# Kernel tuning notes

Measured on AMD Instinct MI355X. Metric: run time of the kernel, lower is better.

## Reference

```python
import jax, jax.numpy as jnp
import numpy as np

H, D = 2, 128            # heads, per-head dim
F_OUT = H * D            # out_channels = 256
N_ADD = 20000
N_DEL = 20000
E = 200000
N_SEL = 4096


def setup_inputs() -> dict:
    key = jax.random.key(0)
    ks = jax.random.split(key, 24)
    p = lambda k, shp: (jax.random.normal(k, shp, dtype=jnp.float32) * 0.05)
    inp = {
        "x_add": jax.random.normal(ks[0], (N_ADD, 768), dtype=jnp.float32),
        "x_del": jax.random.normal(ks[1], (N_DEL, 768), dtype=jnp.float32),
        # per-node-type projections (torch Linear: W [out,in], b [out])
        "W_add": p(ks[2], (F_OUT, 768)), "b_add": p(ks[3], (F_OUT,)),
        "W_del": p(ks[4], (F_OUT, 768)), "b_del": p(ks[5], (F_OUT,)),
        # per-edge-type attention vectors [H, D]
        "att_ad_s": p(ks[6], (H, D)), "att_ad_d": p(ks[7], (H, D)),
        "att_da_s": p(ks[8], (H, D)), "att_da_d": p(ks[9], (H, D)),
        "att_aa_s": p(ks[10], (H, D)), "att_aa_d": p(ks[11], (H, D)),
        "att_dd_s": p(ks[12], (H, D)), "att_dd_d": p(ks[13], (H, D)),
        # semantic attention: k_lin Linear(F_OUT->F_OUT) and query q [F_OUT]
        "k_W": p(ks[14], (F_OUT, F_OUT)), "k_b": p(ks[15], (F_OUT,)),
        "q": p(ks[16], (F_OUT,)),
        # edge indices: row 0 = src node ids, row 1 = dst node ids
        "ei_ad": jax.random.randint(ks[17], (2, E), 0, N_ADD),
        "ei_da": jax.random.randint(ks[18], (2, E), 0, N_DEL),
        "ei_aa": jax.random.randint(ks[19], (2, E), 0, N_ADD),
        "ei_dd": jax.random.randint(ks[20], (2, E), 0, N_DEL),
        "del_idx": jax.random.randint(ks[21], (N_SEL,), 0, N_DEL),
    }
    return inp


def _seg_softmax(a, seg, n):
    # numerically-stable softmax over edges grouped by destination node
    m = jax.ops.segment_max(a, seg, num_segments=n)
    m = jnp.where(jnp.isfinite(m), m, 0.0)
    e = jnp.exp(a - m[seg])
    s = jax.ops.segment_sum(e, seg, num_segments=n)
    return e / (s[seg] + 1e-16)


def _edge_attn(x_src, x_dst, att_s, att_d, ei, n_dst):
    # x_*: [N, H, D]; GAT-style additive attention with leaky_relu(0.2)
    a_s = (x_src * att_s).sum(-1)                   # [Ns, H]
    a_d = (x_dst * att_d).sum(-1)                   # [Nd, H]
    alpha = jax.nn.leaky_relu(a_s[ei[0]] + a_d[ei[1]], 0.2)  # [E, H]
    alpha = _seg_softmax(alpha, ei[1], n_dst)       # [E, H]
    msg = x_src[ei[0]] * alpha[:, :, None]          # [E, H, D]
    out = jax.ops.segment_sum(msg, ei[1], num_segments=n_dst)  # [Nd, H, D]
    return jax.nn.relu(out).reshape(n_dst, F_OUT)


def _group(xs, q, k_W, k_b):
    # semantic (metapath-level) attention
    out = jnp.stack(xs)                              # [M, N, F]
    score = (q * jnp.tanh(out @ k_W.T + k_b).mean(axis=1)).sum(-1)  # [M]
    attn = jax.nn.softmax(score)
    return (attn[:, None, None] * out).sum(0)        # [N, F]


def reference(x_add, x_del, W_add, b_add, W_del, b_del,
              att_ad_s, att_ad_d, att_da_s, att_da_d,
              att_aa_s, att_aa_d, att_dd_s, att_dd_d,
              k_W, k_b, q, ei_ad, ei_da, ei_aa, ei_dd, del_idx):
    ha = (x_add @ W_add.T + b_add).reshape(N_ADD, H, D)
    hd = (x_del @ W_del.T + b_del).reshape(N_DEL, H, D)
    # messages grouped by destination node type
    out_del_ad = _edge_attn(ha, hd, att_ad_s, att_ad_d, ei_ad, N_DEL)
    out_del_dd = _edge_attn(hd, hd, att_dd_s, att_dd_d, ei_dd, N_DEL)
    out_add_da = _edge_attn(hd, ha, att_da_s, att_da_d, ei_da, N_ADD)
    out_add_aa = _edge_attn(ha, ha, att_aa_s, att_aa_d, ei_aa, N_ADD)
    out_del = _group([out_del_ad, out_del_dd], q, k_W, k_b)
    _ = _group([out_add_da, out_add_aa], q, k_W, k_b)  # computed by HANConv, unused downstream
    return out_del[del_idx]  # index_select on del_node
```

## Files before the change

kernel.cpp:

```cpp
#include <hip/hip_runtime.h>
#include <hip/hip_bf16.h>


typedef unsigned short u16;
typedef __attribute__((ext_vector_type(8))) __bf16 bf16x8;
typedef __attribute__((ext_vector_type(4))) float f32x4;
typedef const __attribute__((address_space(1))) unsigned int* gu32p;
typedef __attribute__((address_space(3))) unsigned int* su32p;

__device__ inline float bf2f(u16 u) {
    union { unsigned int i; float f; } c; c.i = ((unsigned int)u) << 16; return c.f;
}
__device__ inline u16 f2bf(float f) {
    union { float f; unsigned int i; } c; c.f = f;
    return (u16)((c.i + 0x7fffu + ((c.i >> 16) & 1u)) >> 16);
}
__device__ inline bf16x8 cvt8(f32x4 a, f32x4 b) {
    bf16x8 r;
    r[0] = (__bf16)a[0]; r[1] = (__bf16)a[1]; r[2] = (__bf16)a[2]; r[3] = (__bf16)a[3];
    r[4] = (__bf16)b[0]; r[5] = (__bf16)b[1]; r[6] = (__bf16)b[2]; r[7] = (__bf16)b[3];
    return r;
}
__device__ inline float fast_tanh(float x) {
    x = fminf(9.f, fmaxf(-9.f, x));
    float t = __expf(2.f * x);
    return (t - 1.f) / (t + 1.f);
}

__global__ __launch_bounds__(256) void prep_count(const float* __restrict__ W0, u16* __restrict__ wb0,
                                                  const float* __restrict__ W1, u16* __restrict__ wb1,
                                                  const float* __restrict__ kW, u16* __restrict__ kwb,
                                                  const int* __restrict__ eiA, int* __restrict__ cntA,
                                                  const int* __restrict__ eiB, int* __restrict__ cntB, int E) {
    int b = blockIdx.x;
    if (b < 224) {
        int idx = b * 256 + threadIdx.x;
        const float* s; u16* d; int i;
        if (idx < 24576)      { s = W0; d = wb0; i = idx; }
        else if (idx < 49152) { s = W1; d = wb1; i = idx - 24576; }
        else                  { s = kW; d = kwb; i = idx - 49152; }
        int e = i * 8;
        *(bf16x8*)(d + e) = cvt8(*(const f32x4*)(s + e), *(const f32x4*)(s + e + 4));
    } else {
        int idx = (b - 224) * 256 + threadIdx.x;
        int which = idx >= E;
        int e = idx - (which ? E : 0);
        if (e >= E) return;
        const int* ei = which ? eiB : eiA;
        int* cnt = which ? cntB : cntA;
        atomicAdd(&cnt[ei[E + e]], 1);
    }
}

__global__ __launch_bounds__(256) void gemm_h2(
    const float* __restrict__ X0, const u16* __restrict__ Wb0,
    const float* __restrict__ b0, u16* __restrict__ H0,
    const float* __restrict__ X1, const u16* __restrict__ Wb1,
    const float* __restrict__ b1, u16* __restrict__ H1,
    const float* __restrict__ w_ads, const float* __restrict__ w_add,
    const float* __restrict__ w_dds, const float* __restrict__ w_ddd,
    float* __restrict__ as_ad, float* __restrict__ ad_ad,
    float* __restrict__ as_dd, float* __restrict__ ad_dd, int M) {
    __shared__ float Af[3][2048];
    __shared__ u16   Bb[3][4096];
    int id = blockIdx.x;
    int which = id >= 626;
    if (which) id -= 626;
    int bm = id >> 1, bn = id & 1;
    const float* X = which ? X1 : X0;
    const u16* Wb = which ? Wb1 : Wb0;
    const float* bias = which ? b1 : b0;
    u16* H = which ? H1 : H0;

    int tid = threadIdx.x;
    int w = tid >> 6, lane = tid & 63;
    int wm = w & 1, wn = w >> 1;
    int row16 = lane & 15, quad = lane >> 4;

#define ISSUE(kt, b) { \
    int kA = (kt) * 32; \
    _Pragma("unroll") \
    for (int j = 0; j < 2; ++j) { \
        int rloc = (w * 2 + j) * 8 + (lane >> 3); \
        int rg = bm * 64 + rloc; if (rg > M - 1) rg = M - 1; \
        int c = (lane & 7) ^ (rloc & 7); \
        const float* gp = X + (size_t)rg * 768 + kA + c * 4; \
        float* lp = Af[b] + (w * 2 + j) * 256; \
        __builtin_amdgcn_global_load_lds((gu32p)(const void*)gp, (su32p)(void*)lp, 16, 0, 0); \
    } \
    _Pragma("unroll") \
    for (int j = 0; j < 2; ++j) { \
        int rloc = (w * 2 + j) * 16 + (lane >> 2); \
        int c = (lane & 3) ^ ((rloc >> 1) & 3); \
        const u16* gp = Wb + (size_t)(bn * 128 + rloc) * 768 + kA + c * 8; \
        u16* lp = Bb[b] + (w * 2 + j) * 512; \
        __builtin_amdgcn_global_load_lds((gu32p)(const void*)gp, (su32p)(void*)lp, 16, 0, 0); \
    } }

    ISSUE(0, 0)
    ISSUE(1, 1)

    f32x4 acc[2][4] = {};
#pragma unroll
    for (int ks = 0; ks < 24; ++ks) {
        int cur = ks % 3;
        if (ks < 23) { asm volatile("s_waitcnt vmcnt(4)" ::: "memory"); }
        else         { asm volatile("s_waitcnt vmcnt(0)" ::: "memory"); }
        asm volatile("s_barrier" ::: "memory");
        if (ks + 2 < 24) { int nb = (ks + 2) % 3; ISSUE(ks + 2, nb) }
        bf16x8 af[2], bv[4];
#pragma unroll
        for (int mi = 0; mi < 2; ++mi) {
            int r = wm * 32 + mi * 16 + row16;
            int c0 = (2 * quad) ^ (r & 7), c1 = (2 * quad + 1) ^ (r & 7);
            f32x4 f0 = *(const f32x4*)(Af[cur] + r * 32 + c0 * 4);
            f32x4 f1 = *(const f32x4*)(Af[cur] + r * 32 + c1 * 4);
            af[mi] = cvt8(f0, f1);
        }
#pragma unroll
        for (int ni = 0; ni < 4; ++ni) {
            int r = wn * 64 + ni * 16 + row16;
            int c = quad ^ ((r >> 1) & 3);
            bv[ni] = *(const bf16x8*)(Bb[cur] + r * 32 + c * 8);
        }
#pragma unroll
        for (int mi = 0; mi < 2; ++mi)
#pragma unroll
            for (int ni = 0; ni < 4; ++ni)
                acc[mi][ni] = __builtin_amdgcn_mfma_f32_16x16x32_bf16(af[mi], bv[ni], acc[mi][ni], 0, 0, 0);
    }
#undef ISSUE

    __syncthreads();
    u16* eps = (u16*)Af;
    const int SE2 = 136;
#pragma unroll
    for (int ni = 0; ni < 4; ++ni) {
        int lcol = wn * 64 + ni * 16 + row16;
        float bvv = bias[bn * 128 + lcol];
#pragma unroll
        for (int mi = 0; mi < 2; ++mi)
#pragma unroll
            for (int r = 0; r < 4; ++r)
                eps[(wm * 32 + mi * 16 + quad * 4 + r) * SE2 + lcol] = f2bf(acc[mi][ni][r] + bvv);
    }
    __syncthreads();
    int mlim = M - bm * 64;
    int c0 = (tid & 15) * 8;
    float wv[3][8];
    int nw = which ? 3 : 1;
    const float* att0 = which ? w_add : w_ads;
    const float* att1 = w_dds;
    const float* att2 = w_ddd;
#pragma unroll
    for (int j = 0; j < 8; ++j) {
        wv[0][j] = att0[bn * 128 + c0 + j];
        wv[1][j] = att1[bn * 128 + c0 + j];
        wv[2][j] = att2[bn * 128 + c0 + j];
    }
#pragma unroll
    for (int p = 0; p < 4; ++p) {
        int row = p * 16 + (tid >> 4);
        uint4 v = *(const uint4*)(eps + row * SE2 + c0);
        if (row < mlim)
            *(uint4*)(H + (size_t)(bm * 64 + row) * 256 + bn * 128 + c0) = v;
        float d0 = 0.f, d1 = 0.f, d2 = 0.f;
#pragma unroll
        for (int j = 0; j < 8; ++j) {
            float hv = bf2f(eps[row * SE2 + c0 + j]);
            d0 += hv * wv[0][j];
            if (which) { d1 += hv * wv[1][j]; d2 += hv * wv[2][j]; }
        }
#pragma unroll
        for (int off = 8; off >= 1; off >>= 1) {
            d0 += __shfl_down(d0, off, 16);
            if (which) { d1 += __shfl_down(d1, off, 16); d2 += __shfl_down(d2, off, 16); }
        }
        if ((tid & 15) == 0 && row < mlim) {
            int n = bm * 64 + row;
            if (!which) {
                unsafeAtomicAdd(&as_ad[n * 2 + bn], d0);
            } else {
                unsafeAtomicAdd(&ad_ad[n * 2 + bn], d0);
                unsafeAtomicAdd(&as_dd[n * 2 + bn], d1);
                unsafeAtomicAdd(&ad_dd[n * 2 + bn], d2);
            }
        }
    }
}

__global__ __launch_bounds__(1024) void scan_two(const int* __restrict__ cntA, int* __restrict__ offA,
                                                 const int* __restrict__ cntB, int* __restrict__ offB, int n) {
    const int* cnt = blockIdx.x ? cntB : cntA;
    int* off = blockIdx.x ? offB : offA;
    __shared__ int wsum[16];
    __shared__ int woff[16];
    __shared__ int tot_s;
    __shared__ int carry_s;
    int tid = threadIdx.x, wid = tid >> 6, lane = tid & 63;
    if (tid == 0) carry_s = 0;
    __syncthreads();
    for (int base = 0; base < n; base += 4096) {
        int i = base + tid * 4;
        int v0 = (i + 0 < n) ? cnt[i + 0] : 0;
        int v1 = (i + 1 < n) ? cnt[i + 1] : 0;
        int v2 = (i + 2 < n) ? cnt[i + 2] : 0;
        int v3 = (i + 3 < n) ? cnt[i + 3] : 0;
        int s0 = v0, s1 = s0 + v1, s2 = s1 + v2, s3 = s2 + v3;
        int x = s3;
#pragma unroll
        for (int d = 1; d < 64; d <<= 1) {
            int t = __shfl_up(x, d, 64);
            if (lane >= d) x += t;
        }
        if (lane == 63) wsum[wid] = x;
        __syncthreads();
        if (wid == 0) {
            int s = (lane < 16) ? wsum[lane] : 0;
#pragma unroll
            for (int d = 1; d < 16; d <<= 1) {
                int t = __shfl_up(s, d, 64);
                if (lane >= d) s += t;
            }
            if (lane < 16) woff[lane] = s - wsum[lane];
            if (lane == 15) tot_s = s;
        }
        __syncthreads();
        int basev = carry_s + woff[wid] + (x - s3);
        if (i + 0 < n) off[i + 0] = basev;
        if (i + 1 < n) off[i + 1] = basev + s0;
        if (i + 2 < n) off[i + 2] = basev + s1;
        if (i + 3 < n) off[i + 3] = basev + s2;
        __syncthreads();
        if (tid == 0) carry_s += tot_s;
    }
    __syncthreads();
    if (tid == 0) off[n] = carry_s;
}

__global__ __launch_bounds__(256) void fill_csr2(const int* __restrict__ eiA, const int* __restrict__ offA,
                                                 int* __restrict__ curA, int* __restrict__ srcsA,
                                                 const int* __restrict__ eiB, const int* __restrict__ offB,
                                                 int* __restrict__ curB, int* __restrict__ srcsB, int E) {
    int idx = blockIdx.x * 256 + threadIdx.x;
    int which = idx >= E;
    int e = idx - (which ? E : 0);
    if (e >= E) return;
    const int* ei = which ? eiB : eiA;
    const int* off = which ? offB : offA;
    int* cursor = which ? curB : curA;
    int* srcs = which ? srcsB : srcsA;
    int s = ei[e], d = ei[E + e];
    int slot = off[d] + atomicAdd(&cursor[d], 1);
    srcs[slot] = s;
}

__global__ __launch_bounds__(256) void edge_gather2(const int* __restrict__ offA, const int* __restrict__ srcsA,
                                                    const float* __restrict__ asA, const float* __restrict__ adA,
                                                    const u16* __restrict__ hA, u16* __restrict__ outA,
                                                    const int* __restrict__ offB, const int* __restrict__ srcsB,
                                                    const float* __restrict__ asB, const float* __restrict__ adB,
                                                    const u16* __restrict__ hB, u16* __restrict__ outB, int N) {
    int gid = blockIdx.x * 256 + threadIdx.x;
    int dall = gid >> 6;
    int which = dall >= N;
    int d = dall - (which ? N : 0);
    if (d >= N) return;
    const int* off = which ? offB : offA;
    const int* srcs = which ? srcsB : srcsA;
    const float* a_src = which ? asB : asA;
    const float* a_dst = which ? adB : adA;
    const u16* h = which ? hB : hA;
    u16* out = which ? outB : outA;
    int lane = gid & 63;
    int hh = lane >> 5;
    int f = lane * 4;
    float ad0 = a_dst[d * 2 + hh];
    int beg = off[d], end = off[d + 1];
    float4 acc = {0.f, 0.f, 0.f, 0.f};
    float S = 0.f;
    int p = beg;
    for (; p + 2 <= end; p += 2) {
        int s0 = srcs[p], s1 = srcs[p + 1];
        ushort4 x0 = *(const ushort4*)(h + (size_t)s0 * 256 + f);
        ushort4 x1 = *(const ushort4*)(h + (size_t)s1 * 256 + f);
        float v0 = a_src[s0 * 2 + hh] + ad0;
        float v1 = a_src[s1 * 2 + hh] + ad0;
        v0 = v0 > 0.f ? v0 : 0.2f * v0;
        v1 = v1 > 0.f ? v1 : 0.2f * v1;
        float e0 = __expf(v0), e1 = __expf(v1);
        S += e0 + e1;
        acc.x += e0 * bf2f(x0.x) + e1 * bf2f(x1.x);
        acc.y += e0 * bf2f(x0.y) + e1 * bf2f(x1.y);
        acc.z += e0 * bf2f(x0.z) + e1 * bf2f(x1.z);
        acc.w += e0 * bf2f(x0.w) + e1 * bf2f(x1.w);
    }
    if (p < end) {
        int s0 = srcs[p];
        ushort4 x0 = *(const ushort4*)(h + (size_t)s0 * 256 + f);
        float v0 = a_src[s0 * 2 + hh] + ad0;
        v0 = v0 > 0.f ? v0 : 0.2f * v0;
        float e0 = __expf(v0);
        S += e0;
        acc.x += e0 * bf2f(x0.x);
        acc.y += e0 * bf2f(x0.y);
        acc.z += e0 * bf2f(x0.z);
        acc.w += e0 * bf2f(x0.w);
    }
    float inv = 1.f / (S + 1e-16f);
    ushort4 o = {f2bf(acc.x * inv), f2bf(acc.y * inv), f2bf(acc.z * inv), f2bf(acc.w * inv)};
    *(ushort4*)(out + (size_t)d * 256 + f) = o;
}

#define SK 264
__global__ __launch_bounds__(256) void kgemm_score2(const u16* __restrict__ outA,
                                                    const u16* __restrict__ outB,
                                                    const u16* __restrict__ kwb,
                                                    const float* __restrict__ kb,
                                                    const float* __restrict__ qv,
                                                    float* __restrict__ score) {
    __shared__ u16 Bs[128 * SK];
    __shared__ float red[4];
    int slot = blockIdx.x >> 8;
    int b = blockIdx.x & 255;
    const u16* outm = slot ? outB : outA;
    int bn = b & 1;
    int bidx = b >> 1;
    int tid = threadIdx.x;
    int w = tid >> 6, lane = tid & 63;
    int row16 = lane & 15, quad = lane >> 4;

#pragma unroll
    for (int i = 0; i < 16; ++i) {
        int c = tid + 256 * i;
        int r = c >> 5, col8 = (c & 31) * 8;
        *(bf16x8*)(Bs + r * SK + col8) = *(const bf16x8*)(kwb + (size_t)(bn * 128 + r) * 256 + col8);
    }
    __syncthreads();

    float kb0 = kb[bn * 128 + w * 32 + row16];
    float qn0 = qv[bn * 128 + w * 32 + row16];
    float kb1 = kb[bn * 128 + w * 32 + 16 + row16];
    float qn1 = qv[bn * 128 + w * 32 + 16 + row16];
    const u16* b0 = Bs + (w * 32 + row16) * SK + quad * 8;
    const u16* b1 = Bs + (w * 32 + 16 + row16) * SK + quad * 8;

    union U { uint4 q; u16 s[8]; bf16x8 v; };
    float p = 0.f;
    for (int mt = bidx; mt < 1250; mt += 128) {
        const u16* arow = outm + (size_t)(mt * 16 + row16) * 256 + quad * 8;
        U a[8];
#pragma unroll
        for (int s8 = 0; s8 < 8; ++s8) a[s8].q = *(const uint4*)(arow + s8 * 32);
        f32x4 acc0 = {0.f,0.f,0.f,0.f}, acc1 = {0.f,0.f,0.f,0.f};
#pragma unroll
        for (int s8 = 0; s8 < 8; ++s8) {
#pragma unroll
            for (int j = 0; j < 8; ++j)
                if (a[s8].s[j] & 0x8000u) a[s8].s[j] = 0;
            bf16x8 bf0 = *(const bf16x8*)(b0 + s8 * 32);
            bf16x8 bf1 = *(const bf16x8*)(b1 + s8 * 32);
            acc0 = __builtin_amdgcn_mfma_f32_16x16x32_bf16(a[s8].v, bf0, acc0, 0, 0, 0);
            acc1 = __builtin_amdgcn_mfma_f32_16x16x32_bf16(a[s8].v, bf1, acc1, 0, 0, 0);
        }
#pragma unroll
        for (int r = 0; r < 4; ++r) {
            p += qn0 * fast_tanh(acc0[r] + kb0);
            p += qn1 * fast_tanh(acc1[r] + kb1);
        }
    }
#pragma unroll
    for (int off = 32; off >= 1; off >>= 1) p += __shfl_down(p, off, 64);
    if (lane == 0) red[w] = p;
    __syncthreads();
    if (tid == 0) unsafeAtomicAdd(&score[slot], red[0] + red[1] + red[2] + red[3]);
}

__global__ __launch_bounds__(256) void final_combine(const u16* __restrict__ out_ad,
                                                     const u16* __restrict__ out_dd,
                                                     const float* __restrict__ score,
                                                     const int* __restrict__ del_idx,
                                                     float* __restrict__ out) {
    int i = blockIdx.x;
    int f = threadIdx.x;
    int node = del_idx[i];
    float s0 = score[0] * (1.f / 20000.f);
    float s1 = score[1] * (1.f / 20000.f);
    float m = fmaxf(s0, s1);
    float e0 = __expf(s0 - m), e1 = __expf(s1 - m);
    float inv = 1.f / (e0 + e1);
    float a0 = e0 * inv, a1 = e1 * inv;
    float v0 = bf2f(out_ad[(size_t)node * 256 + f]); v0 = v0 > 0.f ? v0 : 0.f;
    float v1 = bf2f(out_dd[(size_t)node * 256 + f]); v1 = v1 > 0.f ? v1 : 0.f;
    out[(size_t)i * 256 + f] = a0 * v0 + a1 * v1;
}

extern "C" void kernel_launch(void* const* d_in, const int* in_sizes, int n_in,
                              void* d_out, int out_size, void* d_ws, size_t ws_size,
                              hipStream_t stream) {
    const float* x_add    = (const float*)d_in[0];
    const float* x_del    = (const float*)d_in[1];
    const float* W_add    = (const float*)d_in[2];
    const float* b_add    = (const float*)d_in[3];
    const float* W_del    = (const float*)d_in[4];
    const float* b_del    = (const float*)d_in[5];
    const float* att_ad_s = (const float*)d_in[6];
    const float* att_ad_d = (const float*)d_in[7];
    const float* att_dd_s = (const float*)d_in[12];
    const float* att_dd_d = (const float*)d_in[13];
    const float* k_W      = (const float*)d_in[14];
    const float* k_b      = (const float*)d_in[15];
    const float* q        = (const float*)d_in[16];
    const int* ei_ad      = (const int*)d_in[17];
    const int* ei_dd      = (const int*)d_in[20];
    const int* del_idx    = (const int*)d_in[21];
    float* out = (float*)d_out;

    const int N = 20000, E = 200000;
    char* ws = (char*)d_ws;
    size_t o = 0;
    int* cnt_ad = (int*)(ws + o); o += (size_t)N * 4;
    int* cur_ad = (int*)(ws + o); o += (size_t)N * 4;
    int* cnt_dd = (int*)(ws + o); o += (size_t)N * 4;
    int* cur_dd = (int*)(ws + o); o += (size_t)N * 4;
    float* as_ad = (float*)(ws + o); o += (size_t)N * 2 * 4;
    float* ad_ad = (float*)(ws + o); o += (size_t)N * 2 * 4;
    float* as_dd = (float*)(ws + o); o += (size_t)N * 2 * 4;
    float* ad_dd = (float*)(ws + o); o += (size_t)N * 2 * 4;
    float* score = (float*)(ws + o); o += 256;
    size_t zero_bytes = o;
    u16* wb_add = (u16*)(ws + o); o += (size_t)256 * 768 * 2;
    u16* wb_del = (u16*)(ws + o); o += (size_t)256 * 768 * 2;
    u16* kwb    = (u16*)(ws + o); o += (size_t)256 * 256 * 2;
    int* off_ad = (int*)(ws + o); o += (size_t)(N + 1) * 4;
    int* off_dd = (int*)(ws + o); o += (size_t)(N + 1) * 4;
    int* srcs_ad = (int*)(ws + o); o += (size_t)E * 4;
    int* srcs_dd = (int*)(ws + o); o += (size_t)E * 4;
    u16* out_ad = (u16*)(ws + o); o += (size_t)N * 256 * 2;
    u16* out_dd = (u16*)(ws + o); o += (size_t)N * 256 * 2;
    u16* ha    = (u16*)(ws + o); o += (size_t)N * 256 * 2;
    u16* hd    = (u16*)(ws + o); o += (size_t)N * 256 * 2;

    hipMemsetAsync(d_ws, 0, zero_bytes, stream);

    prep_count<<<224 + (2 * E + 255) / 256, 256, 0, stream>>>(
        W_add, wb_add, W_del, wb_del, k_W, kwb, ei_ad, cnt_ad, ei_dd, cnt_dd, E);
    scan_two<<<2, 1024, 0, stream>>>(cnt_ad, off_ad, cnt_dd, off_dd, N);
    fill_csr2<<<(2 * E + 255) / 256, 256, 0, stream>>>(ei_ad, off_ad, cur_ad, srcs_ad,
                                                       ei_dd, off_dd, cur_dd, srcs_dd, E);

    gemm_h2<<<1252, 256, 0, stream>>>(x_add, wb_add, b_add, ha,
                                      x_del, wb_del, b_del, hd,
                                      att_ad_s, att_ad_d, att_dd_s, att_dd_d,
                                      as_ad, ad_ad, as_dd, ad_dd, N);

    edge_gather2<<<10000, 256, 0, stream>>>(off_ad, srcs_ad, as_ad, ad_ad, ha, out_ad,
                                            off_dd, srcs_dd, as_dd, ad_dd, hd, out_dd, N);

    kgemm_score2<<<512, 256, 0, stream>>>(out_ad, out_dd, kwb, k_b, q, score);
    final_combine<<<4096, 256, 0, stream>>>(out_ad, out_dd, score, del_idx, out);
}
```

Measured before the change: 352.8 us.

## Widen projection GEMM tile to full 256 columns and stage X as bf16 in registers

The node-projection GEMM now uses 512-thread blocks that each compute a 64x256 output tile, so each X row tile is read from global memory once instead of twice (once per column half). X is loaded into registers, converted to bf16 and written to LDS in 128-wide K chunks with double buffering, while W tiles still stream through a triple-buffered async global-to-LDS path. This removes the duplicated fp32 X traffic and the per-step fp32-to-bf16 conversion inside the MFMA loop. In exchange it needs more registers and a hand-tuned waitcnt schedule, and it halves the number of blocks.

Result: faster. 329.3 us (-6.7%).

```diff
diff --git a/kernel.cpp b/kernel.cpp
--- a/kernel.cpp
+++ b/kernel.cpp
@@ -52,7 +52,7 @@
     }
 }
 
-__global__ __launch_bounds__(256) void gemm_h2(
+__global__ __launch_bounds__(512, 4) void gemm_h3(
     const float* __restrict__ X0, const u16* __restrict__ Wb0,
     const float* __restrict__ b0, u16* __restrict__ H0,
     const float* __restrict__ X1, const u16* __restrict__ Wb1,
@@ -61,12 +61,10 @@
     const float* __restrict__ w_dds, const float* __restrict__ w_ddd,
     float* __restrict__ as_ad, float* __restrict__ ad_ad,
     float* __restrict__ as_dd, float* __restrict__ ad_dd, int M) {
-    __shared__ float Af[3][2048];
-    __shared__ u16   Bb[3][4096];
+    __shared__ u16 lds[40960];
     int id = blockIdx.x;
-    int which = id >= 626;
-    if (which) id -= 626;
-    int bm = id >> 1, bn = id & 1;
+    int which = id >= 313;
+    int bm = which ? id - 313 : id;
     const float* X = which ? X1 : X0;
     const u16* Wb = which ? Wb1 : Wb0;
     const float* bias = which ? b1 : b0;
@@ -74,102 +72,131 @@
 
     int tid = threadIdx.x;
     int w = tid >> 6, lane = tid & 63;
-    int wm = w & 1, wn = w >> 1;
+    int wrow = w & 1, wcol = w >> 1;
     int row16 = lane & 15, quad = lane >> 4;
 
-#define ISSUE(kt, b) { \
-    int kA = (kt) * 32; \
-    _Pragma("unroll") \
-    for (int j = 0; j < 2; ++j) { \
-        int rloc = (w * 2 + j) * 8 + (lane >> 3); \
-        int rg = bm * 64 + rloc; if (rg > M - 1) rg = M - 1; \
-        int c = (lane & 7) ^ (rloc & 7); \
-        const float* gp = X + (size_t)rg * 768 + kA + c * 4; \
-        float* lp = Af[b] + (w * 2 + j) * 256; \
-        __builtin_amdgcn_global_load_lds((gu32p)(const void*)gp, (su32p)(void*)lp, 16, 0, 0); \
-    } \
+#define ISSUE_B(kt, slot) { \
     _Pragma("unroll") \
     for (int j = 0; j < 2; ++j) { \
         int rloc = (w * 2 + j) * 16 + (lane >> 2); \
-        int c = (lane & 3) ^ ((rloc >> 1) & 3); \
-        const u16* gp = Wb + (size_t)(bn * 128 + rloc) * 768 + kA + c * 8; \
-        u16* lp = Bb[b] + (w * 2 + j) * 512; \
+        int cc = (lane & 3) ^ ((rloc >> 1) & 3); \
+        const u16* gp = Wb + (size_t)rloc * 768 + (kt) * 32 + cc * 8; \
+        u16* lp = lds + 16384 + (slot) * 8192 + (w * 2 + j) * 512; \
         __builtin_amdgcn_global_load_lds((gu32p)(const void*)gp, (su32p)(void*)lp, 16, 0, 0); \
     } }
 
-    ISSUE(0, 0)
-    ISSUE(1, 1)
+#define ALOAD(c, ar) { \
+    _Pragma("unroll") \
+    for (int i = 0; i < 4; ++i) { \
+        int idx = i * 512 + tid; \
+        int row = idx >> 5, col4 = idx & 31; \
+        int rg = bm * 64 + row; if (rg > M - 1) rg = M - 1; \
+        ar[i] = *(const f32x4*)(X + (size_t)rg * 768 + (c) * 128 + col4 * 4); \
+    } }
+
+#define AWRITE(c, ar) { \
+    _Pragma("unroll") \
+    for (int i = 0; i < 4; ++i) { \
+        int idx = i * 512 + tid; \
+        int row = idx >> 5, col4 = idx & 31; \
+        int off = ((c) & 1) * 8192 + row * 128 + (((col4 >> 1) ^ (row & 7)) << 3) + ((col4 & 1) << 2); \
+        ushort4 v; v.x = f2bf(ar[i][0]); v.y = f2bf(ar[i][1]); v.z = f2bf(ar[i][2]); v.w = f2bf(ar[i][3]); \
+        *(ushort4*)(lds + off) = v; \
+    } }
+
+#define STEP(ks) { \
+    const int ksl = (ks) & 3, buf = ((ks) >> 2) & 1, slot = (ks) % 3; \
+    bf16x8 af[2], bv[4]; \
+    _Pragma("unroll") \
+    for (int mi = 0; mi < 2; ++mi) { \
+        int r = wrow * 32 + mi * 16 + row16; \
+        af[mi] = *(const bf16x8*)(lds + buf * 8192 + r * 128 + (((ksl * 4 + quad) ^ (r & 7)) << 3)); \
+    } \
+    _Pragma("unroll") \
+    for (int ni = 0; ni < 4; ++ni) { \
+        int r = wcol * 64 + ni * 16 + row16; \
+        bv[ni] = *(const bf16x8*)(lds + 16384 + slot * 8192 + r * 32 + ((quad ^ ((r >> 1) & 3)) << 3)); \
+    } \
+    _Pragma("unroll") \
+    for (int mi = 0; mi < 2; ++mi) \
+        _Pragma("unroll") \
+        for (int ni = 0; ni < 4; ++ni) \
+            acc[mi][ni] = __builtin_amdgcn_mfma_f32_16x16x32_bf16(af[mi], bv[ni], acc[mi][ni], 0, 0, 0); \
+}
+
+    f32x4 a0[4], a1[4];
+    ISSUE_B(0, 0)
+    ISSUE_B(1, 1)
+    ALOAD(0, a0)
+    ALOAD(1, a1)
+    asm volatile("s_waitcnt vmcnt(4)" ::: "memory");
+    AWRITE(0, a0)
+    asm volatile("s_waitcnt lgkmcnt(0)" ::: "memory");
+    asm volatile("s_barrier" ::: "memory");
 
     f32x4 acc[2][4] = {};
 #pragma unroll
     for (int ks = 0; ks < 24; ++ks) {
-        int cur = ks % 3;
-        if (ks < 23) { asm volatile("s_waitcnt vmcnt(4)" ::: "memory"); }
-        else         { asm volatile("s_waitcnt vmcnt(0)" ::: "memory"); }
-        asm volatile("s_barrier" ::: "memory");
-        if (ks + 2 < 24) { int nb = (ks + 2) % 3; ISSUE(ks + 2, nb) }
-        bf16x8 af[2], bv[4];
-#pragma unroll
-        for (int mi = 0; mi < 2; ++mi) {
-            int r = wm * 32 + mi * 16 + row16;
-            int c0 = (2 * quad) ^ (r & 7), c1 = (2 * quad + 1) ^ (r & 7);
-            f32x4 f0 = *(const f32x4*)(Af[cur] + r * 32 + c0 * 4);
-            f32x4 f1 = *(const f32x4*)(Af[cur] + r * 32 + c1 * 4);
-            af[mi] = cvt8(f0, f1);
-        }
+        if (ks > 0) {
+            const int wv = (ks == 23) ? 0 : (ks >= 17) ? 2 : ((ks & 2) ? 6 : 2);
+            if (wv == 0)      asm volatile("s_waitcnt vmcnt(0) lgkmcnt(0)" ::: "memory");
+            else if (wv == 2) asm volatile("s_waitcnt vmcnt(2) lgkmcnt(0)" ::: "memory");
+            else              asm volatile("s_waitcnt vmcnt(6) lgkmcnt(0)" ::: "memory");
+            asm volatile("s_barrier" ::: "memory");
+        }
+        if (ks < 22) ISSUE_B(ks + 2, (ks + 2) % 3)
+        if (ks == 0) {
+            asm volatile("s_waitcnt vmcnt(2)" ::: "memory");
+            AWRITE(1, a1)
+        } else if ((ks & 3) == 0 && ks <= 16) {
+            AWRITE(ks / 4 + 1, a0)
+        }
+        if ((ks & 3) == 1 && ks <= 13) ALOAD(ks / 4 + 2, a0)
+        STEP(ks)
+    }
+#undef ISSUE_B
+#undef ALOAD
+#undef AWRITE
+#undef STEP
+
+    __syncthreads();
+    u16* eps = lds;
+    const int SE2 = 264;
+#pragma unroll
+    for (int mi = 0; mi < 2; ++mi)
 #pragma unroll
         for (int ni = 0; ni < 4; ++ni) {
-            int r = wn * 64 + ni * 16 + row16;
-            int c = quad ^ ((r >> 1) & 3);
-            bv[ni] = *(const bf16x8*)(Bb[cur] + r * 32 + c * 8);
-        }
-#pragma unroll
-        for (int mi = 0; mi < 2; ++mi)
-#pragma unroll
-            for (int ni = 0; ni < 4; ++ni)
-                acc[mi][ni] = __builtin_amdgcn_mfma_f32_16x16x32_bf16(af[mi], bv[ni], acc[mi][ni], 0, 0, 0);
-    }
-#undef ISSUE
-
-    __syncthreads();
-    u16* eps = (u16*)Af;
-    const int SE2 = 136;
-#pragma unroll
-    for (int ni = 0; ni < 4; ++ni) {
-        int lcol = wn * 64 + ni * 16 + row16;
-        float bvv = bias[bn * 128 + lcol];
-#pragma unroll
-        for (int mi = 0; mi < 2; ++mi)
+            int col = wcol * 64 + ni * 16 + row16;
+            float bvv = bias[col];
 #pragma unroll
             for (int r = 0; r < 4; ++r)
-                eps[(wm * 32 + mi * 16 + quad * 4 + r) * SE2 + lcol] = f2bf(acc[mi][ni][r] + bvv);
-    }
+                eps[(wrow * 32 + mi * 16 + quad * 4 + r) * SE2 + col] = f2bf(acc[mi][ni][r] + bvv);
+        }
     __syncthreads();
     int mlim = M - bm * 64;
-    int c0 = (tid & 15) * 8;
-    float wv[3][8];
-    int nw = which ? 3 : 1;
+    int c0 = (tid & 31) * 8;
+    int hh = c0 >> 7;
+    float wv0[8], wv1[8], wv2[8];
     const float* att0 = which ? w_add : w_ads;
-    const float* att1 = w_dds;
-    const float* att2 = w_ddd;
 #pragma unroll
     for (int j = 0; j < 8; ++j) {
-        wv[0][j] = att0[bn * 128 + c0 + j];
-        wv[1][j] = att1[bn * 128 + c0 + j];
-        wv[2][j] = att2[bn * 128 + c0 + j];
+        wv0[j] = att0[c0 + j];
+        wv1[j] = w_dds[c0 + j];
+        wv2[j] = w_ddd[c0 + j];
     }
 #pragma unroll
     for (int p = 0; p < 4; ++p) {
-        int row = p * 16 + (tid >> 4);
-        uint4 v = *(const uint4*)(eps + row * SE2 + c0);
+        int row = p * 16 + (tid >> 5);
+        union { uint4 q; u16 s[8]; } v;
+        v.q = *(const uint4*)(eps + row * SE2 + c0);
         if (row < mlim)
-            *(uint4*)(H + (size_t)(bm * 64 + row) * 256 + bn * 128 + c0) = v;
+            *(uint4*)(H + (size_t)(bm * 64 + row) * 256 + c0) = v.q;
         float d0 = 0.f, d1 = 0.f, d2 = 0.f;
 #pragma unroll
         for (int j = 0; j < 8; ++j) {
-            float hv = bf2f(eps[row * SE2 + c0 + j]);
-            d0 += hv * wv[0][j];
-            if (which) { d1 += hv * wv[1][j]; d2 += hv * wv[2][j]; }
+            float hv = bf2f(v.s[j]);
+            d0 += hv * wv0[j];
+            if (which) { d1 += hv * wv1[j]; d2 += hv * wv2[j]; }
         }
 #pragma unroll
         for (int off = 8; off >= 1; off >>= 1) {
@@ -179,11 +206,11 @@
         if ((tid & 15) == 0 && row < mlim) {
             int n = bm * 64 + row;
             if (!which) {
-                unsafeAtomicAdd(&as_ad[n * 2 + bn], d0);
+                unsafeAtomicAdd(&as_ad[n * 2 + hh], d0);
             } else {
-                unsafeAtomicAdd(&ad_ad[n * 2 + bn], d0);
-                unsafeAtomicAdd(&as_dd[n * 2 + bn], d1);
-                unsafeAtomicAdd(&ad_dd[n * 2 + bn], d2);
+                unsafeAtomicAdd(&ad_ad[n * 2 + hh], d0);
+                unsafeAtomicAdd(&as_dd[n * 2 + hh], d1);
+                unsafeAtomicAdd(&ad_dd[n * 2 + hh], d2);
             }
         }
     }
@@ -449,10 +476,10 @@
     fill_csr2<<<(2 * E + 255) / 256, 256, 0, stream>>>(ei_ad, off_ad, cur_ad, srcs_ad,
                                                        ei_dd, off_dd, cur_dd, srcs_dd, E);
 
-    gemm_h2<<<1252, 256, 0, stream>>>(x_add, wb_add, b_add, ha,
-                                      x_del, wb_del, b_del, hd,
-                                      att_ad_s, att_ad_d, att_dd_s, att_dd_d,
-                                      as_ad, ad_ad, as_dd, ad_dd, N);
+    gemm_h3<<<626, 512, 0, stream>>>(x_add, wb_add, b_add, ha,
+                                     x_del, wb_del, b_del, hd,
+                                     att_ad_s, att_ad_d, att_dd_s, att_dd_d,
+                                     as_ad, ad_ad, as_dd, ad_dd, N);
 
     edge_gather2<<<10000, 256, 0, stream>>>(off_ad, srcs_ad, as_ad, ad_ad, ha, out_ad,
                                             off_dd, srcs_dd, as_dd, ad_dd, hd, out_dd, N);
```
